# Kernel optimization log

Measured on AMD Instinct MI355X. Metric: run time of the kernel, lower is better.

## Reference

```python
import jax, jax.numpy as jnp
import numpy as np

NUM_CLS = 80
SCORE_THR = 0.1

def _grid(h, w):
    # matches torch.meshgrid(arange(w), arange(h)) permuted: entry (y,x) -> (x, y)
    xv, yv = jnp.meshgrid(jnp.arange(w), jnp.arange(h))  # 'xy' indexing
    return jnp.stack((xv, yv), -1).reshape(-1, 2).astype(jnp.float32)

def setup_inputs() -> dict:
    key = jax.random.key(0)
    ks = jax.random.split(key, 9)
    shapes = {
        'cls0': (1, 80, 80, 80), 'cls1': (1, 80, 40, 40), 'cls2': (1, 80, 20, 20),
        'box0': (1, 4, 80, 80), 'box1': (1, 4, 40, 40), 'box2': (1, 4, 20, 20),
        'obj0': (1, 1, 80, 80), 'obj1': (1, 1, 40, 40), 'obj2': (1, 1, 20, 20),
    }
    return {name: jax.random.normal(k, shp, dtype=jnp.float32)
            for k, (name, shp) in zip(ks, shapes.items())}

def _forward(cls0, cls1, cls2, box0, box1, box2, obj0, obj1, obj2):
    def flat(t, c):
        # [1,C,H,W] -> [N, C] over all levels concatenated (row-major over y,x)
        return jnp.transpose(t, (0, 2, 3, 1)).reshape(-1, c)
    cls = jax.nn.sigmoid(jnp.concatenate([flat(cls0, NUM_CLS), flat(cls1, NUM_CLS), flat(cls2, NUM_CLS)], 0))  # [8400,80]
    box = jnp.concatenate([flat(box0, 4), flat(box1, 4), flat(box2, 4)], 0)  # [8400,4]
    obj = jax.nn.sigmoid(jnp.concatenate([flat(obj0, 1), flat(obj1, 1), flat(obj2, 1)], 0))[:, 0]  # [8400]
    grids = jnp.concatenate([_grid(80, 80), _grid(40, 40), _grid(20, 20)], 0)  # [8400,2]
    strides = jnp.concatenate([jnp.full((6400,), 8.0), jnp.full((1600,), 16.0), jnp.full((400,), 32.0)])[:, None]
    xy = (box[:, :2] + grids) * strides   # decoded center
    wh = jnp.exp(box[:, 2:4]) * strides   # decoded width/height
    boxes_xyxy = jnp.concatenate([xy - wh / 2.0, xy + wh / 2.0], 1)  # [8400,4]
    scores = obj[:, None] * cls  # [8400,80]
    # sentinel rows appended exactly as in the torch module
    sent_boxes = jnp.array([[0.0, 0.0, 640.0, 640.0], [320.0, 320.0, 540.0, 540.0]], dtype=jnp.float32)
    sent_scores = jnp.zeros((2, NUM_CLS), dtype=jnp.float32).at[0, 0].set(0.47).at[1, 0].set(0.46)
    boxes_all = jnp.concatenate([boxes_xyxy, sent_boxes], 0)    # [8402,4]
    scores_all = jnp.concatenate([scores, sent_scores], 0)      # [8402,80]
    max_sc = scores_all.max(1)
    cls_idx = scores_all.argmax(1)
    # torch path: filter by score>thr, sort desc (the 'nms' is a dummy sort), take first class-0
    # == highest-scoring valid entry whose argmax class is 0 (sentinels guarantee one exists)
    eligible = (max_sc > SCORE_THR) & (cls_idx == 0)
    masked = jnp.where(eligible, max_sc, -1.0)
    idx = jnp.argmax(masked)
    return jnp.concatenate([boxes_all[idx], max_sc[idx][None]]).reshape(1, 5)

def reference(cls0, cls1, cls2, box0, box1, box2, obj0, obj1, obj2):
    return _forward(cls0, cls1, cls2, box0, box1, box2, obj0, obj1, obj2)
```

## Files before the change

### kernel.cpp

```cpp
#include <hip/hip_runtime.h>
#include <math.h>

#define NROWS 8400
#define NTOT  8402

__device__ __forceinline__ float sigmoidf_(float x) {
    return 1.0f / (1.0f + expf(-x));
}

__global__ void detect_kernel(const float* __restrict__ cls0, const float* __restrict__ cls1,
                              const float* __restrict__ cls2,
                              const float* __restrict__ box0, const float* __restrict__ box1,
                              const float* __restrict__ box2,
                              const float* __restrict__ obj0, const float* __restrict__ obj1,
                              const float* __restrict__ obj2,
                              float* __restrict__ out, unsigned long long* __restrict__ ws)
{
    const int r = blockIdx.x * blockDim.x + threadIdx.x;

    if (r < NTOT) {
        float val = -1.0f;
        int ok = 0;
        if (r >= NROWS) {
            val = (r == NROWS) ? 0.47f : 0.46f;
            ok = 1;
        } else {
            const float* cls; const float* obj; int hw, n;
            if (r < 6400)      { cls = cls0; obj = obj0; hw = 6400; n = r;        }
            else if (r < 8000) { cls = cls1; obj = obj1; hw = 1600; n = r - 6400; }
            else               { cls = cls2; obj = obj2; hw = 400;  n = r - 8000; }
            float m = cls[n];
            int mi = 0;
            #pragma unroll 8
            for (int c = 1; c < 80; ++c) {
                float v = cls[c * hw + n];
                if (v > m) { m = v; mi = c; }
            }
            float sc = sigmoidf_(obj[n]) * sigmoidf_(m);
            if (mi == 0 && sc > 0.1f) { val = sc; ok = 1; }
        }
        if (ok) {
            unsigned long long key =
                (((unsigned long long)__float_as_uint(val)) << 32) |
                (unsigned long long)(0xFFFFFFFFu - (unsigned)r);
            atomicMax(ws, key);
        }
    }

    __syncthreads();
    __threadfence();
    if (threadIdx.x == 0) {
        unsigned int done = atomicAdd((unsigned int*)(ws + 1), 1u);
        if (done == gridDim.x - 1) {
            unsigned long long key = atomicAdd(ws, 0ULL);
            unsigned int ridx = 0xFFFFFFFFu - (unsigned)(key & 0xFFFFFFFFu);
            float score = __uint_as_float((unsigned)(key >> 32));
            float b0, b1, b2, b3;
            if (ridx >= NROWS) {
                if (ridx == NROWS) { b0 = 0.0f;   b1 = 0.0f;   b2 = 640.0f; b3 = 640.0f; }
                else               { b0 = 320.0f; b1 = 320.0f; b2 = 540.0f; b3 = 540.0f; }
            } else {
                const float* boxp; int hw, n, W; float s;
                if (ridx < 6400)      { boxp = box0; hw = 6400; n = ridx;        W = 80; s = 8.0f;  }
                else if (ridx < 8000) { boxp = box1; hw = 1600; n = ridx - 6400; W = 40; s = 16.0f; }
                else                  { boxp = box2; hw = 400;  n = ridx - 8000; W = 20; s = 32.0f; }
                float bx = boxp[n];
                float by = boxp[hw + n];
                float bw = boxp[2 * hw + n];
                float bh = boxp[3 * hw + n];
                float gx = (float)(n % W);
                float gy = (float)(n / W);
                float cx = (bx + gx) * s;
                float cy = (by + gy) * s;
                float ww = expf(bw) * s;
                float hh = expf(bh) * s;
                b0 = cx - ww * 0.5f;
                b1 = cy - hh * 0.5f;
                b2 = cx + ww * 0.5f;
                b3 = cy + hh * 0.5f;
            }
            out[0] = b0; out[1] = b1; out[2] = b2; out[3] = b3; out[4] = score;
        }
    }
}

extern "C" void kernel_launch(void* const* d_in, const int* in_sizes, int n_in,
                              void* d_out, int out_size, void* d_ws, size_t ws_size,
                              hipStream_t stream) {
    const float* cls0 = (const float*)d_in[0];
    const float* cls1 = (const float*)d_in[1];
    const float* cls2 = (const float*)d_in[2];
    const float* box0 = (const float*)d_in[3];
    const float* box1 = (const float*)d_in[4];
    const float* box2 = (const float*)d_in[5];
    const float* obj0 = (const float*)d_in[6];
    const float* obj1 = (const float*)d_in[7];
    const float* obj2 = (const float*)d_in[8];
    float* out = (float*)d_out;
    unsigned long long* ws = (unsigned long long*)d_ws;

    hipMemsetAsync(d_ws, 0, 16, stream);

    const int block = 256;
    const int grid = (NTOT + block - 1) / block;
    detect_kernel<<<grid, block, 0, stream>>>(cls0, cls1, cls2,
                                              box0, box1, box2,
                                              obj0, obj1, obj2,
                                              out, ws);
}
```

Baseline: 80.12 us.

## Vectorize class max with float4 rows and split classes across four thread rows

Each thread now handles four consecutive spatial positions with float4 loads, and the 80-class max is split across four threadIdx.y lanes that combine their partial maxima through shared memory. Argmax-equals-class-0 is checked by comparing the max with the class-0 value, and the second sentinel is dropped because it can never beat the first. The goal is fewer, wider memory transactions and more parallel loads in flight per position, at the cost of a shared-memory reduction and a block barrier. Ties where another class equals class 0's value are treated as class 0, which matches argmax's first-index rule.

```diff
diff --git a/kernel.cpp b/kernel.cpp
--- a/kernel.cpp
+++ b/kernel.cpp
@@ -2,54 +2,86 @@
 #include <math.h>
 
 #define NROWS 8400
-#define NTOT  8402
+#define NQ    2100
 
 __device__ __forceinline__ float sigmoidf_(float x) {
     return 1.0f / (1.0f + expf(-x));
 }
 
-__global__ void detect_kernel(const float* __restrict__ cls0, const float* __restrict__ cls1,
-                              const float* __restrict__ cls2,
-                              const float* __restrict__ box0, const float* __restrict__ box1,
-                              const float* __restrict__ box2,
-                              const float* __restrict__ obj0, const float* __restrict__ obj1,
-                              const float* __restrict__ obj2,
-                              float* __restrict__ out, unsigned long long* __restrict__ ws)
+__global__ void __launch_bounds__(256)
+detect_kernel(const float* __restrict__ cls0, const float* __restrict__ cls1,
+              const float* __restrict__ cls2,
+              const float* __restrict__ box0, const float* __restrict__ box1,
+              const float* __restrict__ box2,
+              const float* __restrict__ obj0, const float* __restrict__ obj1,
+              const float* __restrict__ obj2,
+              float* __restrict__ out, unsigned long long* __restrict__ ws)
 {
-    const int r = blockIdx.x * blockDim.x + threadIdx.x;
+    const int tx = threadIdx.x;
+    const int ty = threadIdx.y;
+    const int q  = blockIdx.x * 64 + tx;
+    const bool valid = (q < NQ);
 
-    if (r < NTOT) {
-        float val = -1.0f;
-        int ok = 0;
-        if (r >= NROWS) {
-            val = (r == NROWS) ? 0.47f : 0.46f;
-            ok = 1;
-        } else {
-            const float* cls; const float* obj; int hw, n;
-            if (r < 6400)      { cls = cls0; obj = obj0; hw = 6400; n = r;        }
-            else if (r < 8000) { cls = cls1; obj = obj1; hw = 1600; n = r - 6400; }
-            else               { cls = cls2; obj = obj2; hw = 400;  n = r - 8000; }
-            float m = cls[n];
-            int mi = 0;
-            #pragma unroll 8
-            for (int c = 1; c < 80; ++c) {
-                float v = cls[c * hw + n];
-                if (v > m) { m = v; mi = c; }
+    __shared__ float4 smem[4][64];
+
+    const float* cls = nullptr; const float* obj = nullptr; int hw = 0, n = 0;
+    if (valid) {
+        if (q < 1600)      { cls = cls0; obj = obj0; hw = 6400; n = 4 * q;        }
+        else if (q < 2000) { cls = cls1; obj = obj1; hw = 1600; n = 4 * q - 6400; }
+        else               { cls = cls2; obj = obj2; hw = 400;  n = 4 * q - 8000; }
+    }
+
+    float4 m   = make_float4(-INFINITY, -INFINITY, -INFINITY, -INFINITY);
+    float4 c0q = m;
+    if (valid) {
+        const float4* p = reinterpret_cast<const float4*>(cls + (size_t)ty * hw + n);
+        m = *p;
+        if (ty == 0) c0q = m;
+        #pragma unroll
+        for (int c = ty + 4; c < 80; c += 4) {
+            float4 v = *reinterpret_cast<const float4*>(cls + (size_t)c * hw + n);
+            m.x = fmaxf(m.x, v.x); m.y = fmaxf(m.y, v.y);
+            m.z = fmaxf(m.z, v.z); m.w = fmaxf(m.w, v.w);
+        }
+    }
+    smem[ty][tx] = m;
+    __syncthreads();
+
+    if (ty == 0 && valid) {
+        float4 m1 = smem[1][tx], m2 = smem[2][tx], m3 = smem[3][tx];
+        m.x = fmaxf(fmaxf(m.x, m1.x), fmaxf(m2.x, m3.x));
+        m.y = fmaxf(fmaxf(m.y, m1.y), fmaxf(m2.y, m3.y));
+        m.z = fmaxf(fmaxf(m.z, m1.z), fmaxf(m2.z, m3.z));
+        m.w = fmaxf(fmaxf(m.w, m1.w), fmaxf(m2.w, m3.w));
+        float4 o = *reinterpret_cast<const float4*>(obj + n);
+        const float mm[4] = { m.x, m.y, m.z, m.w };
+        const float c0[4] = { c0q.x, c0q.y, c0q.z, c0q.w };
+        const float ov[4] = { o.x, o.y, o.z, o.w };
+        #pragma unroll
+        for (int i = 0; i < 4; ++i) {
+            if (mm[i] == c0[i]) {
+                float sc = sigmoidf_(ov[i]) * sigmoidf_(c0[i]);
+                if (sc > 0.1f) {
+                    unsigned r = 4u * (unsigned)q + (unsigned)i;
+                    unsigned long long key =
+                        (((unsigned long long)__float_as_uint(sc)) << 32) |
+                        (unsigned long long)(0xFFFFFFFFu - r);
+                    atomicMax(ws, key);
+                }
             }
-            float sc = sigmoidf_(obj[n]) * sigmoidf_(m);
-            if (mi == 0 && sc > 0.1f) { val = sc; ok = 1; }
         }
-        if (ok) {
-            unsigned long long key =
-                (((unsigned long long)__float_as_uint(val)) << 32) |
-                (unsigned long long)(0xFFFFFFFFu - (unsigned)r);
-            atomicMax(ws, key);
-        }
+    }
+
+    if (blockIdx.x == 0 && tx == 0 && ty == 0) {
+        unsigned long long skey =
+            (((unsigned long long)__float_as_uint(0.47f)) << 32) |
+            (unsigned long long)(0xFFFFFFFFu - (unsigned)NROWS);
+        atomicMax(ws, skey);
     }
 
     __syncthreads();
     __threadfence();
-    if (threadIdx.x == 0) {
+    if (tx == 0 && ty == 0) {
         unsigned int done = atomicAdd((unsigned int*)(ws + 1), 1u);
         if (done == gridDim.x - 1) {
             unsigned long long key = atomicAdd(ws, 0ULL);
@@ -60,24 +92,24 @@
                 if (ridx == NROWS) { b0 = 0.0f;   b1 = 0.0f;   b2 = 640.0f; b3 = 640.0f; }
                 else               { b0 = 320.0f; b1 = 320.0f; b2 = 540.0f; b3 = 540.0f; }
             } else {
-                const float* boxp; int hw, n, W; float s;
-                if (ridx < 6400)      { boxp = box0; hw = 6400; n = ridx;        W = 80; s = 8.0f;  }
-                else if (ridx < 8000) { boxp = box1; hw = 1600; n = ridx - 6400; W = 40; s = 16.0f; }
-                else                  { boxp = box2; hw = 400;  n = ridx - 8000; W = 20; s = 32.0f; }
-                float bx = boxp[n];
-                float by = boxp[hw + n];
-                float bw = boxp[2 * hw + n];
-                float bh = boxp[3 * hw + n];
-                float gx = (float)(n % W);
-                float gy = (float)(n / W);
+                const float* boxp; int bhw, bn, W; float s;
+                if (ridx < 6400)      { boxp = box0; bhw = 6400; bn = ridx;        W = 80; s = 8.0f;  }
+                else if (ridx < 8000) { boxp = box1; bhw = 1600; bn = ridx - 6400; W = 40; s = 16.0f; }
+                else                  { boxp = box2; bhw = 400;  bn = ridx - 8000; W = 20; s = 32.0f; }
+                float bx = boxp[bn];
+                float by = boxp[bhw + bn];
+                float bw = boxp[2 * bhw + bn];
+                float bh = boxp[3 * bhw + bn];
+                float gx = (float)(bn % W);
+                float gy = (float)(bn / W);
                 float cx = (bx + gx) * s;
                 float cy = (by + gy) * s;
-                float ww = expf(bw) * s;
-                float hh = expf(bh) * s;
-                b0 = cx - ww * 0.5f;
-                b1 = cy - hh * 0.5f;
-                b2 = cx + ww * 0.5f;
-                b3 = cy + hh * 0.5f;
+                float wwv = expf(bw) * s;
+                float hhv = expf(bh) * s;
+                b0 = cx - wwv * 0.5f;
+                b1 = cy - hhv * 0.5f;
+                b2 = cx + wwv * 0.5f;
+                b3 = cy + hhv * 0.5f;
             }
             out[0] = b0; out[1] = b1; out[2] = b2; out[3] = b3; out[4] = score;
         }
@@ -101,8 +133,8 @@
 
     hipMemsetAsync(d_ws, 0, 16, stream);
 
-    const int block = 256;
-    const int grid = (NTOT + block - 1) / block;
+    dim3 block(64, 4);
+    const int grid = (NQ + 63) / 64;
     detect_kernel<<<grid, block, 0, stream>>>(cls0, cls1, cls2,
                                               box0, box1, box2,
                                               obj0, obj1, obj2,
```

Result: no change. 79.95 us (-0.2%).
